# Kernel optimization log

Measured on AMD Instinct MI355X. Metric: run time of the kernel, lower is better.

The kernel has to match this reference:

```python
import jax, jax.numpy as jnp
import numpy as np

EPS = 1e-8

def squash(t, axis=-1):
    sq = jnp.sum(t * t, axis=axis, keepdims=True)
    scale = sq / (1.0 + sq)
    return scale * t / jnp.sqrt(sq + EPS)

def setup_inputs() -> dict:
    key = jax.random.key(0)
    k1, k2 = jax.random.split(key)
    B, N_IN, D_IN, N_OUT, D_OUT = 256, 1152, 8, 10, 16
    x = jax.random.normal(k1, (B, N_IN, D_IN), dtype=jnp.float32)
    W = 0.01 * jax.random.normal(k2, (1, N_IN, N_OUT, D_OUT, D_IN), dtype=jnp.float32)
    return {"x": x, "W": W}

def reference(x, W):
    # u_hat[b,n,o,j] = sum_i W[0,n,o,j,i] * x[b,n,i]   -> (B, N_in, N_out, D_out)
    u_hat = jnp.einsum('noji,bni->bnoj', W[0], x)
    # b_ij starts with batch dim 1 (as in original torch code) and broadcasts
    b_ij = jnp.zeros((1, u_hat.shape[1], u_hat.shape[2], 1), dtype=u_hat.dtype)
    v_j = None
    for _ in range(3):  # fixed 3 routing iterations
        c_ij = jax.nn.softmax(b_ij, axis=2)            # over output capsules
        s_j = jnp.sum(c_ij * u_hat, axis=1, keepdims=True)  # (B,1,N_out,D_out)
        v_j = squash(s_j, axis=-1)
        b_ij = b_ij + jnp.sum(u_hat * v_j, axis=-1, keepdims=True)
    return jnp.squeeze(v_j, axis=1)  # (B, N_out, D_out)
```

## Files before the change

### kernel.cpp

```cpp
#include <hip/hip_runtime.h>

#define B_ 256
#define N_IN 1152
#define N_OUT 10
#define OJ 160
#define SN (B_*OJ)
#define LOG2E 1.44269504088896340736f
#define NSG 72
#define NPB 16
#define NPW 4
#define NP1 (NSG*16)

typedef __attribute__((ext_vector_type(8))) short bf16x8;
typedef __attribute__((ext_vector_type(4))) float f32x4;

#define NW_ELEMS (N_IN*N_OUT*16)
#define NX_ELEMS (B_*N_IN)
#define NWB (NW_ELEMS/256)

__device__ __forceinline__ unsigned short f2bf(float f) {
  unsigned u = __float_as_uint(f);
  u += 0x7fffu + ((u >> 16) & 1u);
  return (unsigned short)(u >> 16);
}
__device__ __forceinline__ float bf2f(unsigned short s) {
  return __uint_as_float(((unsigned)s) << 16);
}
__device__ __forceinline__ void split8(const float* p, bf16x8& vh, bf16x8& vl) {
  const float4 a = *(const float4*)p;
  const float4 b = *(const float4*)(p + 4);
  const float w[8] = {a.x,a.y,a.z,a.w,b.x,b.y,b.z,b.w};
#pragma unroll
  for (int e=0;e<8;e++){
    unsigned short hh = f2bf(w[e]);
    vh[e] = (short)hh;
    vl[e] = (short)f2bf(w[e] - bf2f(hh));
  }
}

template<int CTRL>
__device__ __forceinline__ float dpp_add(float xx) {
  int y = __builtin_amdgcn_mov_dpp(__float_as_int(xx), CTRL, 0xF, 0xF, false);
  return xx + __int_as_float(y);
}
__device__ __forceinline__ float row_sum16(float xx) {
  xx = dpp_add<0x128>(xx); xx = dpp_add<0x124>(xx);
  xx = dpp_add<0x122>(xx); xx = dpp_add<0x121>(xx);
  return xx;
}
__device__ __forceinline__ float squash_elem(float t) {
  const float sq = row_sum16(t * t);
  return t * (sq / (1.f + sq)) * rsqrtf(sq + 1e-8f);
}

__device__ __forceinline__ void sgbg_map(int bid, int& sg, int& bg) {
  const int xcd = bid & 7, q = bid >> 3;
  sg = xcd*9 + (q >> 4);
  bg = q & 15;
}


__global__ __launch_bounds__(256) void pass1_fused(
    const float* __restrict__ W, const float* __restrict__ x,
    short* __restrict__ WH, short* __restrict__ WL,
    short* __restrict__ XH, short* __restrict__ XL,
    float* __restrict__ P) {
  const int bid = blockIdx.x, tid = threadIdx.x;
  if (bid >= NP1) {
    const int t = (bid - NP1)*256 + tid;
    bf16x8 vh, vl; split8(W + (size_t)t*8, vh, vl);
    ((bf16x8*)WH)[t] = vh; ((bf16x8*)WL)[t] = vl;
    return;
  }
  __shared__ f32x4 red[3*640];
  int sg, bg; sgbg_map(bid, sg, bg);
  const int w = tid >> 6, l = tid & 63;
  const int bb = l & 15, c = l >> 4;
  const int b0 = bg*16, n0 = sg*NPB + w*NPW;
  const bool useLoA = (c & 1) != 0, useLoB = (c >> 1) != 0;

  const f32x4 zz = {0.f,0.f,0.f,0.f};
  f32x4 acc[N_OUT];
#pragma unroll
  for (int o=0;o<N_OUT;o++) acc[o] = zz;

  for (int nn=0; nn<NPW; ++nn) {
    const int n = n0 + nn;
    bf16x8 xh, xl;
    split8(&x[((size_t)(b0+bb)*N_IN + n)*8], xh, xl);
    if (c == 0) ((bf16x8*)XH)[(size_t)n*B_ + b0 + bb] = xh;
    if (c == 2) ((bf16x8*)XL)[(size_t)n*B_ + b0 + bb] = xl;
    const bf16x8 bfrag = useLoB ? xl : xh;
    const float* Wp = &W[(size_t)n*1280 + bb*8];
#pragma unroll
    for (int o=0;o<N_OUT;o++) {
      bf16x8 ah, al;
      split8(Wp + o*128, ah, al);
      const bf16x8 afrag = useLoA ? al : ah;
      acc[o] = __builtin_amdgcn_mfma_f32_16x16x32_bf16(afrag, bfrag, acc[o], 0,0,0);
    }
  }

  if (w) {
#pragma unroll
    for (int o=0;o<N_OUT;o++) red[(w-1)*640 + o*64 + l] = acc[o];
  }
  __syncthreads();
  if (!w) {
    float* Pp = &P[(size_t)sg*SN + (size_t)(b0+bb)*OJ + c*4];
#pragma unroll
    for (int o=0;o<N_OUT;o++) {
      acc[o] += red[o*64+l] + red[640+o*64+l] + red[1280+o*64+l];
      *(f32x4*)&Pp[o*16] = acc[o];
    }
  }
}

__global__ __launch_bounds__(256) void caps_pass23(
    const short* __restrict__ WH, const short* __restrict__ WL,
    const short* __restrict__ XH, const short* __restrict__ XL,
    const float* __restrict__ veff, float* __restrict__ P) {
  __shared__ f32x4 red[3*640];
  int sg, bg; sgbg_map(blockIdx.x, sg, bg);
  const int tid = threadIdx.x, w = tid >> 6, l = tid & 63;
  const int bb = l & 15, c = l >> 4;
  const int b0 = bg*16;
  const int n0 = sg*NPB + w*NPW;
  const short* Abase = (c & 1)  ? WL : WH;
  const short* Bbase = (c >> 1) ? XL : XH;

  const f32x4 zz = {0.f,0.f,0.f,0.f};
  f32x4 acc[N_OUT], vj[N_OUT];
  const float* vp = &veff[(size_t)(b0+bb)*OJ + c*4];
#pragma unroll
  for (int o=0;o<N_OUT;o++) { vj[o] = *(const f32x4*)&vp[o*16]; acc[o] = zz; }

  for (int nn=0; nn<NPW; ++nn) {
    const int n = n0 + nn;
    const bf16x8 bfrag = *(const bf16x8*)&Bbase[((size_t)n*B_ + b0 + bb)*8];
    const short* Ap = &Abase[(size_t)n*1280 + bb*8];
    f32x4 u[N_OUT];
#pragma unroll
    for (int o=0;o<N_OUT;o++) {
      const bf16x8 afrag = *(const bf16x8*)&Ap[o*128];
      u[o] = __builtin_amdgcn_mfma_f32_16x16x32_bf16(afrag, bfrag, zz, 0,0,0);
    }
    float ez[N_OUT], Z = 0.f;
#pragma unroll
    for (int o=0;o<N_OUT;o++) {
      float t = u[o][0]*vj[o][0] + u[o][1]*vj[o][1]
              + u[o][2]*vj[o][2] + u[o][3]*vj[o][3];
      t += __shfl_xor(t, 16);
      t += __shfl_xor(t, 32);
      ez[o] = exp2f(t);
      Z += ez[o];
    }
    const float invZ = 1.f / Z;
#pragma unroll
    for (int o=0;o<N_OUT;o++) acc[o] += (ez[o]*invZ) * u[o];
  }

  if (w) {
#pragma unroll
    for (int o=0;o<N_OUT;o++) red[(w-1)*640 + o*64 + l] = acc[o];
  }
  __syncthreads();
  if (!w) {
    float* Pp = &P[(size_t)sg*SN + (size_t)(b0+bb)*OJ + c*4];
#pragma unroll
    for (int o=0;o<N_OUT;o++) {
      acc[o] += red[o*64+l] + red[640+o*64+l] + red[1280+o*64+l];
      *(f32x4*)&Pp[o*16] = acc[o];
    }
  }
}

__global__ __launch_bounds__(256) void caps_finish(const float* __restrict__ P, float scale,
                                                   const float* __restrict__ vprev,
                                                   float* __restrict__ vout, float lscale) {
  const int idx = blockIdx.x*256 + threadIdx.x;
  float t = 0.f;
#pragma unroll 8
  for (int g=0; g<NSG; ++g) t += P[(size_t)g*SN + idx];
  t *= scale;
  float v = squash_elem(t) * lscale;
  if (vprev != nullptr) v += vprev[idx];
  vout[idx] = v;
}

extern "C" void kernel_launch(void* const* d_in, const int* in_sizes, int n_in,
                              void* d_out, int out_size, void* d_ws, size_t ws_size,
                              hipStream_t stream) {
  const float* x = (const float*)d_in[0];
  const float* W = (const float*)d_in[1];
  float* out = (float*)d_out;

  float* P   = (float*)d_ws;
  float* v1  = P  + (size_t)NSG*SN;
  float* v12 = v1 + SN;
  short* WH = (short*)(v12 + SN);
  short* WL = WH + (size_t)NW_ELEMS*8;
  short* XH = WL + (size_t)NW_ELEMS*8;
  short* XL = XH + (size_t)NX_ELEMS*8;

  pass1_fused<<<NP1 + NWB, 256, 0, stream>>>(W, x, WH, WL, XH, XL, P);
  caps_finish<<<SN/256, 256, 0, stream>>>(P, 0.1f, nullptr, v1, LOG2E);
  caps_pass23<<<NP1, 256, 0, stream>>>(WH, WL, XH, XL, v1, P);
  caps_finish<<<SN/256, 256, 0, stream>>>(P, 1.0f, v1, v12, LOG2E);
  caps_pass23<<<NP1, 256, 0, stream>>>(WH, WL, XH, XL, v12, P);
  caps_finish<<<SN/256, 256, 0, stream>>>(P, 1.0f, nullptr, out, 1.0f);
}
```

Measured before the change: 97.83 us.

## Split packing from pass1, halve per-block N slice, tree-reduce partials

Moves the bf16 hi/lo packing of x into a separate pack kernel that transposes through LDS. Pass1 becomes a pure MFMA kernel that reads the packed data. Each block now covers 8 input capsules instead of 16, so the grid doubles to 144x16 blocks and there are more waves to fill the GPU. Cross-wave reduction becomes a two-level tree with extra barriers, and the XCD-aware block mapping is dropped. The trade-off is twice as many partial slices for caps_finish to sum, plus one extra kernel launch.

```diff
diff --git a/kernel.cpp b/kernel.cpp
--- a/kernel.cpp
+++ b/kernel.cpp
@@ -6,10 +6,9 @@
 #define OJ 160
 #define SN (B_*OJ)
 #define LOG2E 1.44269504088896340736f
-#define NSG 72
-#define NPB 16
-#define NPW 4
-#define NP1 (NSG*16)
+#define NPB 8
+#define NPW 2
+#define NSG (N_IN/NPB)
 
 typedef __attribute__((ext_vector_type(8))) short bf16x8;
 typedef __attribute__((ext_vector_type(4))) float f32x4;
@@ -17,6 +16,7 @@
 #define NW_ELEMS (N_IN*N_OUT*16)
 #define NX_ELEMS (B_*N_IN)
 #define NWB (NW_ELEMS/256)
+#define NTILES ((N_IN/16)*(B_/16))
 
 __device__ __forceinline__ unsigned short f2bf(float f) {
   unsigned u = __float_as_uint(f);
@@ -53,77 +53,102 @@
   return t * (sq / (1.f + sq)) * rsqrtf(sq + 1e-8f);
 }
 
-__device__ __forceinline__ void sgbg_map(int bid, int& sg, int& bg) {
-  const int xcd = bid & 7, q = bid >> 3;
-  sg = xcd*9 + (q >> 4);
-  bg = q & 15;
-}
-
-
-__global__ __launch_bounds__(256) void pass1_fused(
-    const float* __restrict__ W, const float* __restrict__ x,
-    short* __restrict__ WH, short* __restrict__ WL,
-    short* __restrict__ XH, short* __restrict__ XL,
-    float* __restrict__ P) {
+__global__ __launch_bounds__(256) void pack_all(const float* __restrict__ W,
+                                                const float* __restrict__ x,
+                                                short* __restrict__ WH, short* __restrict__ WL,
+                                                short* __restrict__ XH, short* __restrict__ XL) {
   const int bid = blockIdx.x, tid = threadIdx.x;
-  if (bid >= NP1) {
-    const int t = (bid - NP1)*256 + tid;
+  if (bid < NWB) {
+    const int t = bid*256 + tid;
     bf16x8 vh, vl; split8(W + (size_t)t*8, vh, vl);
     ((bf16x8*)WH)[t] = vh; ((bf16x8*)WL)[t] = vl;
-    return;
-  }
-  __shared__ f32x4 red[3*640];
-  int sg, bg; sgbg_map(bid, sg, bg);
-  const int w = tid >> 6, l = tid & 63;
+  } else {
+    __shared__ bf16x8 TH[16*17], TL[16*17];
+    const int tile = bid - NWB;
+    const int nt = tile >> 4, bt = tile & 15;
+    const int nn = tid & 15, bb = tid >> 4;
+    bf16x8 vh, vl;
+    split8(x + ((size_t)(bt*16+bb)*N_IN + nt*16+nn)*8, vh, vl);
+    TH[nn*17 + bb] = vh; TL[nn*17 + bb] = vl;
+    __syncthreads();
+    const int bb2 = tid & 15, nn2 = tid >> 4;
+    const size_t o = (size_t)(nt*16+nn2)*B_ + bt*16 + bb2;
+    ((bf16x8*)XH)[o] = TH[nn2*17 + bb2];
+    ((bf16x8*)XL)[o] = TL[nn2*17 + bb2];
+  }
+}
+
+
+__device__ __forceinline__ void tree_and_store(f32x4 (&acc)[N_OUT],
+                                               f32x4 (*red)[640],
+                                               int w, int l, int sg, int b0,
+                                               int bb, int c,
+                                               float* __restrict__ P) {
+  if (w >= 2) {
+#pragma unroll
+    for (int o=0;o<N_OUT;o++) red[w-2][o*64 + l] = acc[o];
+  }
+  __syncthreads();
+  if (w < 2) {
+#pragma unroll
+    for (int o=0;o<N_OUT;o++) acc[o] += red[w][o*64 + l];
+  }
+  __syncthreads();
+  if (w == 1) {
+#pragma unroll
+    for (int o=0;o<N_OUT;o++) red[0][o*64 + l] = acc[o];
+  }
+  __syncthreads();
+  if (w == 0) {
+    float* Pp = &P[(size_t)sg*SN + (size_t)(b0+bb)*OJ + c*4];
+#pragma unroll
+    for (int o=0;o<N_OUT;o++) {
+      acc[o] += red[0][o*64 + l];
+      *(f32x4*)&Pp[o*16] = acc[o];
+    }
+  }
+}
+
+__global__ __launch_bounds__(256) void caps_pass1(
+    const short* __restrict__ WH, const short* __restrict__ WL,
+    const short* __restrict__ XH, const short* __restrict__ XL,
+    float* __restrict__ P) {
+  __shared__ f32x4 red[2][640];
+  const int tid = threadIdx.x, w = tid >> 6, l = tid & 63;
   const int bb = l & 15, c = l >> 4;
-  const int b0 = bg*16, n0 = sg*NPB + w*NPW;
-  const bool useLoA = (c & 1) != 0, useLoB = (c >> 1) != 0;
+  const int sg = blockIdx.x, bg = blockIdx.y;
+  const int b0 = bg*16;
+  const int n0 = sg*NPB + w*NPW;
+  const short* Abase = (c & 1)  ? WL : WH;
+  const short* Bbase = (c >> 1) ? XL : XH;
 
   const f32x4 zz = {0.f,0.f,0.f,0.f};
   f32x4 acc[N_OUT];
 #pragma unroll
   for (int o=0;o<N_OUT;o++) acc[o] = zz;
 
+#pragma unroll
   for (int nn=0; nn<NPW; ++nn) {
     const int n = n0 + nn;
-    bf16x8 xh, xl;
-    split8(&x[((size_t)(b0+bb)*N_IN + n)*8], xh, xl);
-    if (c == 0) ((bf16x8*)XH)[(size_t)n*B_ + b0 + bb] = xh;
-    if (c == 2) ((bf16x8*)XL)[(size_t)n*B_ + b0 + bb] = xl;
-    const bf16x8 bfrag = useLoB ? xl : xh;
-    const float* Wp = &W[(size_t)n*1280 + bb*8];
-#pragma unroll
-    for (int o=0;o<N_OUT;o++) {
-      bf16x8 ah, al;
-      split8(Wp + o*128, ah, al);
-      const bf16x8 afrag = useLoA ? al : ah;
+    const bf16x8 bfrag = *(const bf16x8*)&Bbase[((size_t)n*B_ + b0 + bb)*8];
+    const short* Ap = &Abase[(size_t)n*1280 + bb*8];
+#pragma unroll
+    for (int o=0;o<N_OUT;o++) {
+      const bf16x8 afrag = *(const bf16x8*)&Ap[o*128];
       acc[o] = __builtin_amdgcn_mfma_f32_16x16x32_bf16(afrag, bfrag, acc[o], 0,0,0);
     }
   }
-
-  if (w) {
-#pragma unroll
-    for (int o=0;o<N_OUT;o++) red[(w-1)*640 + o*64 + l] = acc[o];
-  }
-  __syncthreads();
-  if (!w) {
-    float* Pp = &P[(size_t)sg*SN + (size_t)(b0+bb)*OJ + c*4];
-#pragma unroll
-    for (int o=0;o<N_OUT;o++) {
-      acc[o] += red[o*64+l] + red[640+o*64+l] + red[1280+o*64+l];
-      *(f32x4*)&Pp[o*16] = acc[o];
-    }
-  }
+  tree_and_store(acc, red, w, l, sg, b0, bb, c, P);
 }
 
 __global__ __launch_bounds__(256) void caps_pass23(
     const short* __restrict__ WH, const short* __restrict__ WL,
     const short* __restrict__ XH, const short* __restrict__ XL,
     const float* __restrict__ veff, float* __restrict__ P) {
-  __shared__ f32x4 red[3*640];
-  int sg, bg; sgbg_map(blockIdx.x, sg, bg);
+  __shared__ f32x4 red[2][640];
   const int tid = threadIdx.x, w = tid >> 6, l = tid & 63;
   const int bb = l & 15, c = l >> 4;
+  const int sg = blockIdx.x, bg = blockIdx.y;
   const int b0 = bg*16;
   const int n0 = sg*NPB + w*NPW;
   const short* Abase = (c & 1)  ? WL : WH;
@@ -135,6 +160,7 @@
 #pragma unroll
   for (int o=0;o<N_OUT;o++) { vj[o] = *(const f32x4*)&vp[o*16]; acc[o] = zz; }
 
+#pragma unroll
   for (int nn=0; nn<NPW; ++nn) {
     const int n = n0 + nn;
     const bf16x8 bfrag = *(const bf16x8*)&Bbase[((size_t)n*B_ + b0 + bb)*8];
@@ -159,20 +185,7 @@
 #pragma unroll
     for (int o=0;o<N_OUT;o++) acc[o] += (ez[o]*invZ) * u[o];
   }
-
-  if (w) {
-#pragma unroll
-    for (int o=0;o<N_OUT;o++) red[(w-1)*640 + o*64 + l] = acc[o];
-  }
-  __syncthreads();
-  if (!w) {
-    float* Pp = &P[(size_t)sg*SN + (size_t)(b0+bb)*OJ + c*4];
-#pragma unroll
-    for (int o=0;o<N_OUT;o++) {
-      acc[o] += red[o*64+l] + red[640+o*64+l] + red[1280+o*64+l];
-      *(f32x4*)&Pp[o*16] = acc[o];
-    }
-  }
+  tree_and_store(acc, red, w, l, sg, b0, bb, c, P);
 }
 
 __global__ __launch_bounds__(256) void caps_finish(const float* __restrict__ P, float scale,
@@ -203,10 +216,16 @@
   short* XH = WL + (size_t)NW_ELEMS*8;
   short* XL = XH + (size_t)NX_ELEMS*8;
 
-  pass1_fused<<<NP1 + NWB, 256, 0, stream>>>(W, x, WH, WL, XH, XL, P);
+  pack_all<<<NWB + NTILES, 256, 0, stream>>>(W, x, WH, WL, XH, XL);
+
+  const dim3 pg(NSG, 16), pb(256);
+
+  caps_pass1<<<pg, pb, 0, stream>>>(WH, WL, XH, XL, P);
   caps_finish<<<SN/256, 256, 0, stream>>>(P, 0.1f, nullptr, v1, LOG2E);
-  caps_pass23<<<NP1, 256, 0, stream>>>(WH, WL, XH, XL, v1, P);
+
+  caps_pass23<<<pg, pb, 0, stream>>>(WH, WL, XH, XL, v1, P);
   caps_finish<<<SN/256, 256, 0, stream>>>(P, 1.0f, v1, v12, LOG2E);
-  caps_pass23<<<NP1, 256, 0, stream>>>(WH, WL, XH, XL, v12, P);
+
+  caps_pass23<<<pg, pb, 0, stream>>>(WH, WL, XH, XL, v12, P);
   caps_finish<<<SN/256, 256, 0, stream>>>(P, 1.0f, nullptr, out, 1.0f);
 }
```

After: 101.0 us. 3.2% more time.
